# Kernel tuning notes

Measured on AMD Instinct MI355X. Metric: run time of the kernel, lower is better.

Reference implementation:

```python
import jax, jax.numpy as jnp
from jax import lax
import numpy as np

V, E, H, B, T = 512, 512, 1024, 128, 512

def _xavier(key, shape):
    fan_out, fan_in = shape
    bound = float(np.sqrt(6.0 / (fan_in + fan_out)))
    return jax.random.uniform(key, shape, jnp.float32, -bound, bound)

def setup_inputs() -> dict:
    key = jax.random.key(0)
    ks = jax.random.split(key, 6)
    src = jax.random.randint(ks[0], (B, T), 0, V, dtype=jnp.int32)
    embedding = _xavier(ks[1], (V, E))
    w_ih_l0 = _xavier(ks[2], (3 * H, E))
    w_hh_l0 = _xavier(ks[3], (3 * H, H))
    w_ih_l1 = _xavier(ks[4], (3 * H, H))
    w_hh_l1 = _xavier(ks[5], (3 * H, H))
    zb = jnp.zeros((3 * H,), jnp.float32)  # biases init'd to 0 in module
    return {
        "src": src, "embedding": embedding,
        "w_ih_l0": w_ih_l0, "w_hh_l0": w_hh_l0, "b_ih_l0": zb, "b_hh_l0": zb,
        "w_ih_l1": w_ih_l1, "w_hh_l1": w_hh_l1, "b_ih_l1": zb, "b_hh_l1": zb,
    }

def _gru_layer(x_seq, w_ih, w_hh, b_ih, b_hh):
    # x_seq: [B, T, D]. Precompute all input projections as one big GEMM.
    gates_x = jnp.einsum('btd,gd->btg', x_seq, w_ih) + b_ih  # [B, T, 3H]
    h_dim = w_hh.shape[1]
    w_hh_t = w_hh.T  # [H, 3H]

    def step(h, gx):
        gh = h @ w_hh_t + b_hh                      # [B, 3H]
        xr, xz, xn = jnp.split(gx, 3, axis=-1)
        hr, hz, hn = jnp.split(gh, 3, axis=-1)
        r = jax.nn.sigmoid(xr + hr)
        z = jax.nn.sigmoid(xz + hz)
        n = jnp.tanh(xn + r * hn)
        h_new = (1.0 - z) * n + z * h
        return h_new, h_new

    h0 = jnp.zeros((x_seq.shape[0], h_dim), x_seq.dtype)
    h_last, outs = lax.scan(step, h0, jnp.swapaxes(gates_x, 0, 1))  # time-major scan
    return jnp.swapaxes(outs, 0, 1), h_last  # [B, T, H], [B, H]

def reference(src, embedding, w_ih_l0, w_hh_l0, b_ih_l0, b_hh_l0,
              w_ih_l1, w_hh_l1, b_ih_l1, b_hh_l1):
    x = embedding[src]  # [B, T, E]
    y0, h0 = _gru_layer(x, w_ih_l0, w_hh_l0, b_ih_l0, b_hh_l0)
    _, h1 = _gru_layer(y0, w_ih_l1, w_hh_l1, b_ih_l1, b_hh_l1)
    return jnp.stack([h0, h1], axis=0)  # (n_layers, B, H)
```

## Files before the change

kernel.cpp:

```cpp
#include <hip/hip_runtime.h>

typedef __attribute__((ext_vector_type(8))) short short8;
typedef __attribute__((ext_vector_type(4))) float f32x4;
typedef __attribute__((ext_vector_type(2))) unsigned long long u64x2;

constexpr int Bsz = 128;
constexpr int Tlen = 512;
constexpr int Hd = 1024;
constexpr int K1 = 2048;

__device__ __forceinline__ unsigned short f2b(float f) {
  unsigned int u = __float_as_uint(f);
  u = (u + 0x7FFFu + ((u >> 16) & 1u)) >> 16;
  return (unsigned short)u;
}
__device__ __forceinline__ unsigned long long aload64(const unsigned long long* p) {
  return __hip_atomic_load(p, __ATOMIC_RELAXED, __HIP_MEMORY_SCOPE_AGENT);
}
__device__ __forceinline__ unsigned int aload32(const unsigned int* p) {
  return __hip_atomic_load(p, __ATOMIC_RELAXED, __HIP_MEMORY_SCOPE_AGENT);
}
__device__ __forceinline__ void astore32(unsigned int* p, unsigned int v) {
  __hip_atomic_store(p, v, __ATOMIC_RELAXED, __HIP_MEMORY_SCOPE_AGENT);
}

template <int LAYER>
__device__ __forceinline__ void run_layer(
    const int* __restrict__ src, const float* __restrict__ P,
    const unsigned short* __restrict__ Wh, const unsigned short* __restrict__ Wx,
    const float* __restrict__ bhh, const float* __restrict__ bih,
    float* __restrict__ dout, unsigned short* __restrict__ Ab,
    unsigned short* __restrict__ A1,
    unsigned int* __restrict__ flags,
    f32x4 (*__restrict__ red)[3][4][64],
    const int R0, const int J0, const int w, const int lane)
{
  constexpr int KSZ = LAYER ? 2048 : 1024;
  constexpr int KW = KSZ / 4;
  constexpr int NK = KW / 32;
  constexpr int PD = 6;

  const int lrow = lane >> 4;
  const int lcol = lane & 15;
  const int col = J0 + lcol;

  const float bhr = bhh[col], bhz = bhh[1024 + col], bhn = bhh[2048 + col];
  float gbr = 0.f, gbz = 0.f, gbn = 0.f;
  if (LAYER) { gbr = bih[col]; gbz = bih[1024 + col]; gbn = bih[2048 + col]; }

  short8 wB[3][NK];
  {
    const int kw0 = w * KW + lrow * 8;
#pragma unroll
    for (int ks = 0; ks < NK; ++ks) {
      const int k0 = kw0 + ks * 32;
      const unsigned short* ws;
      if (LAYER && k0 >= 1024) ws = Wx + (k0 - 1024);
      else                     ws = Wh + k0;
#pragma unroll
      for (int g = 0; g < 3; ++g)
        wB[g][ks] = *(const short8*)(ws + (g * 1024 + col) * 1024);
    }
  }

  const int myrow0 = R0 + w * 16 + lrow * 4;
  float hold[4] = {0.f, 0.f, 0.f, 0.f};

  for (int r = 0; r <= 512; ++r) {
    const bool active = LAYER ? (r >= 1) : (r < 512);
    if (active) {
      const bool first = LAYER ? (r == 1) : (r == 0);
      const int par = r & 1;
      const unsigned short* Acur = Ab + par * (Bsz * KSZ);
      unsigned short* Anext = Ab + (par ^ 1) * (Bsz * KSZ);
      const bool skipG = first && (LAYER == 0 || w < 2);

      float gpr[4], gpz[4], gpn[4];
      int sv[4];
      if (LAYER == 0) {
#pragma unroll
        for (int i = 0; i < 4; ++i) sv[i] = src[(myrow0 + i) * Tlen + r];
      } else {
#pragma unroll
        for (int i = 0; i < 4; ++i) { gpr[i] = gbr; gpz[i] = gbz; gpn[i] = gbn; }
      }

      f32x4 ar[4], az[4], an[4];
#pragma unroll
      for (int f = 0; f < 4; ++f) {
        ar[f] = (f32x4){0.f, 0.f, 0.f, 0.f};
        az[f] = (f32x4){0.f, 0.f, 0.f, 0.f};
        an[f] = (f32x4){0.f, 0.f, 0.f, 0.f};
      }

      u64x2 abuf[PD][4];
      const unsigned short* abase[4];
      if (!skipG) {
#pragma unroll
        for (int f = 0; f < 4; ++f)
          abase[f] = Acur + (R0 + f * 16 + lcol) * KSZ + w * KW + lrow * 8;
#pragma unroll
        for (int ks = 0; ks < PD; ++ks) {
#pragma unroll
          for (int f = 0; f < 4; ++f) {
            const unsigned long long* ap =
                (const unsigned long long*)(abase[f] + ks * 32);
            abuf[ks][f][0] = aload64(ap);
            abuf[ks][f][1] = aload64(ap + 1);
          }
        }
      }
      if (LAYER == 0) {
#pragma unroll
        for (int i = 0; i < 4; ++i) {
          const float* pr = P + sv[i] * 3072 + col;
          gpr[i] = pr[0]; gpz[i] = pr[1024]; gpn[i] = pr[2048];
        }
      }
      if (!skipG) {
#pragma unroll
        for (int ks = 0; ks < NK; ++ks) {
#pragma unroll
          for (int f = 0; f < 4; ++f) {
            const short8 a = *(const short8*)&abuf[ks % PD][f];
            ar[f] = __builtin_amdgcn_mfma_f32_16x16x32_bf16(a, wB[0][ks], ar[f], 0, 0, 0);
            az[f] = __builtin_amdgcn_mfma_f32_16x16x32_bf16(a, wB[1][ks], az[f], 0, 0, 0);
            an[f] = __builtin_amdgcn_mfma_f32_16x16x32_bf16(a, wB[2][ks], an[f], 0, 0, 0);
          }
          if (ks + PD < NK) {
#pragma unroll
            for (int f = 0; f < 4; ++f) {
              const unsigned long long* ap =
                  (const unsigned long long*)(abase[f] + (ks + PD) * 32);
              abuf[(ks + PD) % PD][f][0] = aload64(ap);
              abuf[(ks + PD) % PD][f][1] = aload64(ap + 1);
            }
          }
        }
      }

#pragma unroll
      for (int f = 0; f < 4; ++f) {
        if (f != w) {
          red[w][0][f][lane] = ar[f];
          red[w][1][f][lane] = az[f];
          red[w][2][f][lane] = an[f];
        }
      }
      __syncthreads();
      f32x4 sr  = (f32x4){0.f, 0.f, 0.f, 0.f};
      f32x4 sz  = (f32x4){0.f, 0.f, 0.f, 0.f};
      f32x4 snh = (f32x4){0.f, 0.f, 0.f, 0.f};
      f32x4 snx = (f32x4){0.f, 0.f, 0.f, 0.f};
      const bool ownH = (LAYER == 0) || (w < 2);
#pragma unroll
      for (int f = 0; f < 4; ++f) {
        if (f == w) {
          sr = ar[f]; sz = az[f];
          if (ownH) snh = an[f]; else snx = an[f];
        }
      }
#pragma unroll
      for (int ww = 0; ww < 4; ++ww) {
        if (ww != w) {
          sr += red[ww][0][w][lane];
          sz += red[ww][1][w][lane];
          const f32x4 nn = red[ww][2][w][lane];
          if (LAYER == 0 || ww < 2) snh += nn; else snx += nn;
        }
      }

      const bool lastw = LAYER ? (r == 512) : (r == 511);
#pragma unroll
      for (int i = 0; i < 4; ++i) {
        const int row = myrow0 + i;
        float rg = sr[i] + gpr[i] + bhr;
        rg = 1.f / (1.f + __expf(-rg));
        float zg = sz[i] + gpz[i] + bhz;
        zg = 1.f / (1.f + __expf(-zg));
        const float nx = (snx[i] + gpn[i]) + rg * (snh[i] + bhn);
        const float e2 = __expf(2.f * fabsf(nx));
        const float ng = copysignf(1.f - 2.f / (e2 + 1.f), nx);
        const float hnew = (1.f - zg) * ng + zg * hold[i];
        hold[i] = hnew;
        const unsigned int hb = (unsigned int)f2b(hnew);
        const unsigned int nb = (unsigned int)__shfl_down((int)hb, 1, 64);
        if ((lcol & 1) == 0) {
          const unsigned int pv = hb | (nb << 16);
          astore32((unsigned int*)(Anext + row * KSZ + J0 + lcol), pv);
          if (LAYER == 0)
            astore32((unsigned int*)(A1 + (par ^ 1) * (Bsz * K1) +
                                     row * K1 + 1024 + J0 + lcol), pv);
        }
        if (lastw) dout[LAYER * (Bsz * Hd) + row * Hd + col] = hnew;
      }
    }

    if (r < 512) {
      __syncthreads();
      if (w == 0) {
        const unsigned tgt = (unsigned)(r + 1);
        if (lane == 0) astore32(&flags[(unsigned)blockIdx.x * 16u], tgt);
        for (;;) {
          const unsigned m0 = aload32(&flags[(unsigned)(lane)       * 16u]);
          const unsigned m1 = aload32(&flags[(unsigned)(lane + 64)  * 16u]);
          const unsigned m2 = aload32(&flags[(unsigned)(lane + 128) * 16u]);
          const unsigned m3 = aload32(&flags[(unsigned)(lane + 192) * 16u]);
          if (__all(m0 >= tgt && m1 >= tgt && m2 >= tgt && m3 >= tgt)) break;
          __builtin_amdgcn_s_sleep(2);
        }
      }
      __syncthreads();
    }
  }
}

__global__ void __launch_bounds__(256, 1) gru_persist(
    const int* __restrict__ src,
    const float* __restrict__ P,
    const unsigned short* __restrict__ Whh0b,
    const unsigned short* __restrict__ Whh1b,
    const unsigned short* __restrict__ Wih1b,
    const float* __restrict__ bhh0,
    const float* __restrict__ bih1,
    const float* __restrict__ bhh1,
    float* __restrict__ dout,
    unsigned short* __restrict__ A0,
    unsigned short* __restrict__ A1,
    unsigned int* __restrict__ flags,
    int* __restrict__ taken)
{
  __shared__ f32x4 red[4][3][4][64];
  __shared__ int s_work;

  const int tid = threadIdx.x;

  if (tid == 0) {
    unsigned int xcc;
    asm volatile("s_getreg_b32 %0, hwreg(HW_REG_XCC_ID)" : "=s"(xcc));
    const int pref = ((int)(xcc & 7u)) * 32;
    int got = -1;
    for (int j = 0; j < 256; ++j) {
      const int idx = (pref + j) & 255;
      int expected = 0;
      if (__hip_atomic_compare_exchange_strong(&taken[idx], &expected, 1,
              __ATOMIC_RELAXED, __ATOMIC_RELAXED, __HIP_MEMORY_SCOPE_AGENT)) {
        got = idx; break;
      }
    }
    s_work = got;
  }
  __syncthreads();
  const int work = s_work;
  const int xcd_w = work >> 5;
  const int slot = work & 31;
  const int layer = (slot >> 4) & 1;
  const int c = xcd_w * 8 + ((slot >> 1) & 7);
  const int mh = slot & 1;
  const int R0 = mh * 64;
  const int J0 = c * 16;

  const int w = tid >> 6;
  const int lane = tid & 63;

  if (layer == 0)
    run_layer<0>(src, P, Whh0b, Wih1b, bhh0, bih1, dout, A0, A1, flags, red,
                 R0, J0, w, lane);
  else
    run_layer<1>(src, P, Whh1b, Wih1b, bhh1, bih1, dout, A1, A1, flags, red,
                 R0, J0, w, lane);
}

__global__ void __launch_bounds__(256) cvt_k(const float* __restrict__ s,
                                            unsigned short* __restrict__ d, int n) {
  const int i = (blockIdx.x * 256 + threadIdx.x) * 8;
  if (i >= n) return;
  const float4 a = *(const float4*)(s + i);
  const float4 b = *(const float4*)(s + i + 4);
  short8 o;
  o[0] = (short)f2b(a.x); o[1] = (short)f2b(a.y);
  o[2] = (short)f2b(a.z); o[3] = (short)f2b(a.w);
  o[4] = (short)f2b(b.x); o[5] = (short)f2b(b.y);
  o[6] = (short)f2b(b.z); o[7] = (short)f2b(b.w);
  *(short8*)(d + i) = o;
}

__global__ void __launch_bounds__(256) pemb_k(const float* __restrict__ emb,
                                             const float* __restrict__ wih0,
                                             const float* __restrict__ bih0,
                                             float* __restrict__ P) {
  __shared__ float se[64 * 64];
  const int g = blockIdx.x * 256 + threadIdx.x;
  const int v0 = blockIdx.y * 64;
  float acc[64];
#pragma unroll
  for (int i = 0; i < 64; ++i) acc[i] = 0.f;
  for (int kb = 0; kb < 8; ++kb) {
    __syncthreads();
#pragma unroll
    for (int s = 0; s < 4; ++s) {
      const int idx = threadIdx.x + s * 256;
      const int vv = idx >> 4, k4 = (idx & 15) * 4;
      *(float4*)(se + vv * 64 + k4) =
          *(const float4*)(emb + (v0 + vv) * 512 + kb * 64 + k4);
    }
    __syncthreads();
    float4 wv[16];
#pragma unroll
    for (int j = 0; j < 16; ++j)
      wv[j] = *(const float4*)(wih0 + g * 512 + kb * 64 + j * 4);
    for (int vv = 0; vv < 64; ++vv) {
      const float* er = se + vv * 64;
      float s0 = acc[vv];
#pragma unroll
      for (int j = 0; j < 16; ++j) {
        const float4 e = *(const float4*)(er + j * 4);
        s0 += wv[j].x * e.x + wv[j].y * e.y + wv[j].z * e.z + wv[j].w * e.w;
      }
      acc[vv] = s0;
    }
  }
  const float bb = bih0[g];
  for (int vv = 0; vv < 64; ++vv) P[(v0 + vv) * 3072 + g] = acc[vv] + bb;
}

__global__ void zero_k(unsigned int* flags, int* taken) {
  const int i = threadIdx.x;
  for (int j = 0; j < 16; ++j) flags[i * 16 + j] = 0u;
  taken[i] = 0;
}

extern "C" void kernel_launch(void* const* d_in, const int* in_sizes, int n_in,
                              void* d_out, int out_size, void* d_ws, size_t ws_size,
                              hipStream_t stream) {
  const int* src = (const int*)d_in[0];
  const float* emb = (const float*)d_in[1];
  const float* wih0 = (const float*)d_in[2];
  const float* whh0 = (const float*)d_in[3];
  const float* bih0 = (const float*)d_in[4];
  const float* bhh0 = (const float*)d_in[5];
  const float* wih1 = (const float*)d_in[6];
  const float* whh1 = (const float*)d_in[7];
  const float* bih1 = (const float*)d_in[8];
  const float* bhh1 = (const float*)d_in[9];
  float* dout = (float*)d_out;

  char* p = (char*)d_ws;
  unsigned short* A0 = (unsigned short*)p;
  unsigned short* A1 = (unsigned short*)(p + 524288);
  unsigned short* Whh0b = (unsigned short*)(p + 1572864);
  unsigned short* Whh1b = (unsigned short*)(p + 7864320);
  unsigned short* Wih1b = (unsigned short*)(p + 14155776);
  float* P = (float*)(p + 20447232);
  unsigned int* flags = (unsigned int*)(p + 26738688);
  int* taken = (int*)(p + 26755072);

  constexpr int NW = 3072 * 1024;
  hipLaunchKernelGGL(cvt_k, dim3(NW / (256 * 8)), dim3(256), 0, stream, whh0, Whh0b, NW);
  hipLaunchKernelGGL(cvt_k, dim3(NW / (256 * 8)), dim3(256), 0, stream, whh1, Whh1b, NW);
  hipLaunchKernelGGL(cvt_k, dim3(NW / (256 * 8)), dim3(256), 0, stream, wih1, Wih1b, NW);
  hipLaunchKernelGGL(pemb_k, dim3(12, 8), dim3(256), 0, stream, emb, wih0, bih0, P);
  hipLaunchKernelGGL(zero_k, dim3(1), dim3(256), 0, stream, flags, taken);

  hipLaunchKernelGGL(gru_persist, dim3(256), dim3(256), 0, stream,
                     src, P, Whh0b, Whh1b, Wih1b, bhh0, bih1, bhh1,
                     dout, A0, A1, flags, taken);
}
```

Baseline: 9.518 ms.

## Split K per warp across Wh and Wx, stream Wx weights, use plain A loads

```diff
diff --git a/kernel.cpp b/kernel.cpp
--- a/kernel.cpp
+++ b/kernel.cpp
@@ -1,8 +1,8 @@
 #include <hip/hip_runtime.h>
+#include <type_traits>
 
 typedef __attribute__((ext_vector_type(8))) short short8;
 typedef __attribute__((ext_vector_type(4))) float f32x4;
-typedef __attribute__((ext_vector_type(2))) unsigned long long u64x2;
 
 constexpr int Bsz = 128;
 constexpr int Tlen = 512;
@@ -13,9 +13,6 @@
   unsigned int u = __float_as_uint(f);
   u = (u + 0x7FFFu + ((u >> 16) & 1u)) >> 16;
   return (unsigned short)u;
-}
-__device__ __forceinline__ unsigned long long aload64(const unsigned long long* p) {
-  return __hip_atomic_load(p, __ATOMIC_RELAXED, __HIP_MEMORY_SCOPE_AGENT);
 }
 __device__ __forceinline__ unsigned int aload32(const unsigned int* p) {
   return __hip_atomic_load(p, __ATOMIC_RELAXED, __HIP_MEMORY_SCOPE_AGENT);
@@ -32,13 +29,16 @@
     float* __restrict__ dout, unsigned short* __restrict__ Ab,
     unsigned short* __restrict__ A1,
     unsigned int* __restrict__ flags,
-    f32x4 (*__restrict__ red)[3][4][64],
+    f32x4 (*__restrict__ red)[4][3][64],
     const int R0, const int J0, const int w, const int lane)
 {
   constexpr int KSZ = LAYER ? 2048 : 1024;
-  constexpr int KW = KSZ / 4;
-  constexpr int NK = KW / 32;
-  constexpr int PD = 6;
+  constexpr int NKH = 8;
+  constexpr int NKX = LAYER ? 8 : 0;
+  constexpr int KE  = NKH + NKX;
+  constexpr int PD  = 3;
+  constexpr int PW  = 4;
+  constexpr int NQ  = LAYER ? 4 : 3;
 
   const int lrow = lane >> 4;
   const int lcol = lane & 15;
@@ -48,19 +48,19 @@
   float gbr = 0.f, gbz = 0.f, gbn = 0.f;
   if (LAYER) { gbr = bih[col]; gbz = bih[1024 + col]; gbn = bih[2048 + col]; }
 
-  short8 wB[3][NK];
-  {
-    const int kw0 = w * KW + lrow * 8;
-#pragma unroll
-    for (int ks = 0; ks < NK; ++ks) {
-      const int k0 = kw0 + ks * 32;
-      const unsigned short* ws;
-      if (LAYER && k0 >= 1024) ws = Wx + (k0 - 1024);
-      else                     ws = Wh + k0;
-#pragma unroll
-      for (int g = 0; g < 3; ++g)
-        wB[g][ks] = *(const short8*)(ws + (g * 1024 + col) * 1024);
-    }
+  short8 wBh[3][NKH];
+#pragma unroll
+  for (int g = 0; g < 3; ++g) {
+    const unsigned short* wp = Wh + (g * 1024 + col) * 1024 + w * 256 + lrow * 8;
+#pragma unroll
+    for (int ks = 0; ks < NKH; ++ks)
+      wBh[g][ks] = *(const short8*)(wp + ks * 32);
+  }
+  const unsigned short* wxp[3];
+  if (LAYER) {
+#pragma unroll
+    for (int g = 0; g < 3; ++g)
+      wxp[g] = Wx + (g * 1024 + col) * 1024 + w * 256 + lrow * 8;
   }
 
   const int myrow0 = R0 + w * 16 + lrow * 4;
@@ -73,100 +73,123 @@
       const int par = r & 1;
       const unsigned short* Acur = Ab + par * (Bsz * KSZ);
       unsigned short* Anext = Ab + (par ^ 1) * (Bsz * KSZ);
-      const bool skipG = first && (LAYER == 0 || w < 2);
+
+      short8 wx[LAYER ? PW : 1][3];
+      if (LAYER) {
+#pragma unroll
+        for (int j = 0; j < PW; ++j)
+#pragma unroll
+          for (int g = 0; g < 3; ++g)
+            wx[j][g] = *(const short8*)(wxp[g] + j * 32);
+      }
 
       float gpr[4], gpz[4], gpn[4];
-      int sv[4];
       if (LAYER == 0) {
+        int sv[4];
 #pragma unroll
         for (int i = 0; i < 4; ++i) sv[i] = src[(myrow0 + i) * Tlen + r];
-      } else {
-#pragma unroll
-        for (int i = 0; i < 4; ++i) { gpr[i] = gbr; gpz[i] = gbz; gpn[i] = gbn; }
-      }
-
-      f32x4 ar[4], az[4], an[4];
-#pragma unroll
-      for (int f = 0; f < 4; ++f) {
-        ar[f] = (f32x4){0.f, 0.f, 0.f, 0.f};
-        az[f] = (f32x4){0.f, 0.f, 0.f, 0.f};
-        an[f] = (f32x4){0.f, 0.f, 0.f, 0.f};
-      }
-
-      u64x2 abuf[PD][4];
-      const unsigned short* abase[4];
-      if (!skipG) {
-#pragma unroll
-        for (int f = 0; f < 4; ++f)
-          abase[f] = Acur + (R0 + f * 16 + lcol) * KSZ + w * KW + lrow * 8;
-#pragma unroll
-        for (int ks = 0; ks < PD; ++ks) {
-#pragma unroll
-          for (int f = 0; f < 4; ++f) {
-            const unsigned long long* ap =
-                (const unsigned long long*)(abase[f] + ks * 32);
-            abuf[ks][f][0] = aload64(ap);
-            abuf[ks][f][1] = aload64(ap + 1);
-          }
-        }
-      }
-      if (LAYER == 0) {
 #pragma unroll
         for (int i = 0; i < 4; ++i) {
           const float* pr = P + sv[i] * 3072 + col;
           gpr[i] = pr[0]; gpz[i] = pr[1024]; gpn[i] = pr[2048];
         }
-      }
-      if (!skipG) {
-#pragma unroll
-        for (int ks = 0; ks < NK; ++ks) {
+      } else {
+#pragma unroll
+        for (int i = 0; i < 4; ++i) { gpr[i] = gbr; gpz[i] = gbz; gpn[i] = gbn; }
+      }
+
+      f32x4 ar[4], az[4], anh[4], anx[4];
+#pragma unroll
+      for (int f = 0; f < 4; ++f) {
+        ar[f]  = (f32x4){0.f, 0.f, 0.f, 0.f};
+        az[f]  = (f32x4){0.f, 0.f, 0.f, 0.f};
+        anh[f] = (f32x4){0.f, 0.f, 0.f, 0.f};
+        anx[f] = (f32x4){0.f, 0.f, 0.f, 0.f};
+      }
+
+      const unsigned short* rowb[4];
+#pragma unroll
+      for (int f = 0; f < 4; ++f)
+        rowb[f] = Acur + (R0 + f * 16 + lcol) * KSZ + w * 256 + lrow * 8;
+
+      auto kloop = [&](auto kbv) {
+        constexpr int kb = decltype(kbv)::value;
+        short8 abuf[PD][4];
+#pragma unroll
+        for (int s = 0; s < PD; ++s) {
+          const int ks = kb + s;
+          if (ks < KE) {
+#pragma unroll
+            for (int f = 0; f < 4; ++f)
+              abuf[s][f] = *(const short8*)(
+                  rowb[f] + ks * 32 + ((LAYER && ks >= NKH) ? 768 : 0));
+          }
+        }
+#pragma unroll
+        for (int ks = kb; ks < KE; ++ks) {
+          short8 br, bz, bn;
+          if (ks < NKH) { br = wBh[0][ks]; bz = wBh[1][ks]; bn = wBh[2][ks]; }
+          else {
+            br = wx[(ks - NKH) % PW][0];
+            bz = wx[(ks - NKH) % PW][1];
+            bn = wx[(ks - NKH) % PW][2];
+          }
 #pragma unroll
           for (int f = 0; f < 4; ++f) {
-            const short8 a = *(const short8*)&abuf[ks % PD][f];
-            ar[f] = __builtin_amdgcn_mfma_f32_16x16x32_bf16(a, wB[0][ks], ar[f], 0, 0, 0);
-            az[f] = __builtin_amdgcn_mfma_f32_16x16x32_bf16(a, wB[1][ks], az[f], 0, 0, 0);
-            an[f] = __builtin_amdgcn_mfma_f32_16x16x32_bf16(a, wB[2][ks], an[f], 0, 0, 0);
-          }
-          if (ks + PD < NK) {
-#pragma unroll
-            for (int f = 0; f < 4; ++f) {
-              const unsigned long long* ap =
-                  (const unsigned long long*)(abase[f] + (ks + PD) * 32);
-              abuf[(ks + PD) % PD][f][0] = aload64(ap);
-              abuf[(ks + PD) % PD][f][1] = aload64(ap + 1);
+            const short8 a = abuf[(ks - kb) % PD][f];
+            ar[f] = __builtin_amdgcn_mfma_f32_16x16x32_bf16(a, br, ar[f], 0, 0, 0);
+            az[f] = __builtin_amdgcn_mfma_f32_16x16x32_bf16(a, bz, az[f], 0, 0, 0);
+            if (ks < NKH)
+              anh[f] = __builtin_amdgcn_mfma_f32_16x16x32_bf16(a, bn, anh[f], 0, 0, 0);
+            else
+              anx[f] = __builtin_amdgcn_mfma_f32_16x16x32_bf16(a, bn, anx[f], 0, 0, 0);
+          }
+          const int kn = ks + PD;
+          if (kn < KE) {
+#pragma unroll
+            for (int f = 0; f < 4; ++f)
+              abuf[(ks - kb) % PD][f] = *(const short8*)(
+                  rowb[f] + kn * 32 + ((LAYER && kn >= NKH) ? 768 : 0));
+          }
+          if (LAYER && ks >= NKH) {
+            const int jn = (ks - NKH) + PW;
+            if (jn < NKX) {
+#pragma unroll
+              for (int g = 0; g < 3; ++g)
+                wx[(ks - NKH) % PW][g] = *(const short8*)(wxp[g] + jn * 32);
             }
           }
         }
-      }
+      };
+      if (!first) kloop(std::integral_constant<int, 0>{});
+      else if (NKX > 0) kloop(std::integral_constant<int, NKH>{});
 
 #pragma unroll
       for (int f = 0; f < 4; ++f) {
         if (f != w) {
-          red[w][0][f][lane] = ar[f];
-          red[w][1][f][lane] = az[f];
-          red[w][2][f][lane] = an[f];
+          const int sl = (f < w) ? f : f - 1;
+          red[w][0][sl][lane] = ar[f];
+          red[w][1][sl][lane] = az[f];
+          red[w][2][sl][lane] = anh[f];
+          if (NQ == 4) red[w][3][sl][lane] = anx[f];
         }
       }
       __syncthreads();
       f32x4 sr  = (f32x4){0.f, 0.f, 0.f, 0.f};
-      f32x4 sz  = (f32x4){0.f, 0.f, 0.f, 0.f};
+      f32x4 sz_ = (f32x4){0.f, 0.f, 0.f, 0.f};
       f32x4 snh = (f32x4){0.f, 0.f, 0.f, 0.f};
       f32x4 snx = (f32x4){0.f, 0.f, 0.f, 0.f};
-      const bool ownH = (LAYER == 0) || (w < 2);
-#pragma unroll
-      for (int f = 0; f < 4; ++f) {
-        if (f == w) {
-          sr = ar[f]; sz = az[f];
-          if (ownH) snh = an[f]; else snx = an[f];
-        }
-      }
+#pragma unroll
+      for (int f = 0; f < 4; ++f)
+        if (f == w) { sr = ar[f]; sz_ = az[f]; snh = anh[f]; if (NQ == 4) snx = anx[f]; }
 #pragma unroll
       for (int ww = 0; ww < 4; ++ww) {
         if (ww != w) {
-          sr += red[ww][0][w][lane];
-          sz += red[ww][1][w][lane];
-          const f32x4 nn = red[ww][2][w][lane];
-          if (LAYER == 0 || ww < 2) snh += nn; else snx += nn;
+          const int sl = (w < ww) ? w : w - 1;
+          sr  += red[ww][0][sl][lane];
+          sz_ += red[ww][1][sl][lane];
+          snh += red[ww][2][sl][lane];
+          if (NQ == 4) snx += red[ww][3][sl][lane];
         }
       }
 
@@ -176,7 +199,7 @@
         const int row = myrow0 + i;
         float rg = sr[i] + gpr[i] + bhr;
         rg = 1.f / (1.f + __expf(-rg));
-        float zg = sz[i] + gpz[i] + bhz;
+        float zg = sz_[i] + gpz[i] + bhz;
         zg = 1.f / (1.f + __expf(-zg));
         const float nx = (snx[i] + gpn[i]) + rg * (snh[i] + bhn);
         const float e2 = __expf(2.f * fabsf(nx));
@@ -207,8 +230,9 @@
           const unsigned m2 = aload32(&flags[(unsigned)(lane + 128) * 16u]);
           const unsigned m3 = aload32(&flags[(unsigned)(lane + 192) * 16u]);
           if (__all(m0 >= tgt && m1 >= tgt && m2 >= tgt && m3 >= tgt)) break;
-          __builtin_amdgcn_s_sleep(2);
-        }
+          __builtin_amdgcn_s_sleep(1);
+        }
+        __builtin_amdgcn_fence(__ATOMIC_ACQUIRE, "agent");
       }
       __syncthreads();
     }
@@ -230,7 +254,7 @@
     unsigned int* __restrict__ flags,
     int* __restrict__ taken)
 {
-  __shared__ f32x4 red[4][3][4][64];
+  __shared__ f32x4 red[4][4][3][64];
   __shared__ int s_work;
 
   const int tid = threadIdx.x;
```

After: 10.90 ms. 1.14x slower.
